# Performance work log

Measured on AMD Instinct MI355X. Metric: run time of the kernel, lower is better.

The kernel has to match this reference:

```python
import jax, jax.numpy as jnp
import numpy as np

D = 512; H = 8; DFF = 2048; S1 = 1024; S2 = 512; B = 8; EPS = 1e-5


def setup_inputs() -> dict:
    key = jax.random.key(0)
    ks = jax.random.split(key, 10)
    def w(k, shape):
        return jax.random.normal(k, shape, dtype=jnp.float32) * 0.02
    return {
        "rna_embed": jax.random.normal(ks[0], (S1, B, D), dtype=jnp.float32),
        "protein_embed": jax.random.normal(ks[1], (S2, B, D), dtype=jnp.float32),
        # self-attention params (torch MHA packed in_proj)
        "Wqkv_s": w(ks[2], (3 * D, D)), "bqkv_s": jnp.zeros((3 * D,), jnp.float32),
        "Wo_s": w(ks[3], (D, D)), "bo_s": jnp.zeros((D,), jnp.float32),
        # cross-attention params
        "Wqkv_c": w(ks[4], (3 * D, D)), "bqkv_c": jnp.zeros((3 * D,), jnp.float32),
        "Wo_c": w(ks[5], (D, D)), "bo_c": jnp.zeros((D,), jnp.float32),
        # FFN params
        "W1": w(ks[6], (DFF, D)), "b1": jnp.zeros((DFF,), jnp.float32),
        "W2": w(ks[7], (D, DFF)), "b2": jnp.zeros((D,), jnp.float32),
        # LayerNorm params: norm0_1, norm1_1, norm1_2, norm2
        "g0": jnp.ones((D,), jnp.float32), "be0": jnp.zeros((D,), jnp.float32),
        "g11": jnp.ones((D,), jnp.float32), "be11": jnp.zeros((D,), jnp.float32),
        "g12": jnp.ones((D,), jnp.float32), "be12": jnp.zeros((D,), jnp.float32),
        "g2": jnp.ones((D,), jnp.float32), "be2": jnp.zeros((D,), jnp.float32),
    }


def _layernorm(x, g, b):
    m = jnp.mean(x, axis=-1, keepdims=True)
    v = jnp.mean(jnp.square(x - m), axis=-1, keepdims=True)
    return (x - m) * jax.lax.rsqrt(v + EPS) * g + b


def _mha(xq, xkv, Wqkv, bqkv, Wo, bo):
    # xq: (Sq, B, D), xkv: (Sk, B, D)
    Wq, Wk, Wv = jnp.split(Wqkv, 3, axis=0)
    bq, bk, bv = jnp.split(bqkv, 3)
    hd = D // H
    scale = 1.0 / np.sqrt(hd).astype(np.float32)
    q = (xq @ Wq.T + bq).reshape(xq.shape[0], -1, H, hd)   # (Sq,B,H,hd)
    k = (xkv @ Wk.T + bk).reshape(xkv.shape[0], -1, H, hd)  # (Sk,B,H,hd)
    v = (xkv @ Wv.T + bv).reshape(xkv.shape[0], -1, H, hd)
    scores = jnp.einsum('qbhd,kbhd->bhqk', q, k) * scale    # (B,H,Sq,Sk)
    attn = jax.nn.softmax(scores, axis=-1)
    o = jnp.einsum('bhqk,kbhd->qbhd', attn, v).reshape(xq.shape[0], -1, D)
    return o @ Wo.T + bo


def reference(rna_embed, protein_embed, Wqkv_s, bqkv_s, Wo_s, bo_s,
              Wqkv_c, bqkv_c, Wo_c, bo_c, W1, b1, W2, b2,
              g0, be0, g11, be11, g12, be12, g2, be2):
    x1 = rna_embed
    # pre-norm self-attention
    h = _layernorm(x1, g0, be0)
    x1 = x1 + _mha(h, h, Wqkv_s, bqkv_s, Wo_s, bo_s)
    # pre-norm cross-attention (queries from x1, keys/values from protein)
    x1 = x1 + _mha(_layernorm(x1, g11, be11), _layernorm(protein_embed, g12, be12),
                   Wqkv_c, bqkv_c, Wo_c, bo_c)
    # pre-norm FFN
    h = _layernorm(x1, g2, be2)
    x1 = x1 + (jax.nn.relu(h @ W1.T + b1) @ W2.T + b2)
    return x1
```

## Files before the change

kernel.cpp:

```cpp
#include <hip/hip_runtime.h>

typedef unsigned short u16;
typedef unsigned int u32;
typedef u16 u16x8 __attribute__((ext_vector_type(8)));
typedef u16 u16x4 __attribute__((ext_vector_type(4)));
typedef short bfx8 __attribute__((ext_vector_type(8)));
typedef float f32x4 __attribute__((ext_vector_type(4)));

#define AS1 __attribute__((address_space(1)))
#define AS3 __attribute__((address_space(3)))

__device__ __forceinline__ u16 f2bf(float f) {
  union { float f; u32 u; } c; c.f = f;
  u32 u = c.u;
  u += 0x7fffu + ((u >> 16) & 1u);
  return (u16)(u >> 16);
}

__device__ __forceinline__ u32 cvt_pk_bf16(float lo, float hi) {
  u32 r;
  asm("v_cvt_pk_bf16_f32 %0, %1, %2" : "=v"(r) : "v"(lo), "v"(hi));
  return r;
}

__device__ __forceinline__ float fexp2(float x) {
  float r;
  asm("v_exp_f32 %0, %1" : "=v"(r) : "v"(x));
  return r;
}

__device__ __forceinline__ void ln_row(const float* __restrict__ x,
                                       const float* __restrict__ g,
                                       const float* __restrict__ be,
                                       u16* __restrict__ out, int gw, int lane) {
  const float4* row = (const float4*)(x + (size_t)gw * 512);
  float4 a = row[2 * lane], b = row[2 * lane + 1];
  float s = a.x + a.y + a.z + a.w + b.x + b.y + b.z + b.w;
  float q = a.x*a.x + a.y*a.y + a.z*a.z + a.w*a.w + b.x*b.x + b.y*b.y + b.z*b.z + b.w*b.w;
#pragma unroll
  for (int m = 1; m < 64; m <<= 1) { s += __shfl_xor(s, m); q += __shfl_xor(q, m); }
  float mean = s * (1.f / 512.f);
  float var = q * (1.f / 512.f) - mean * mean;
  float rs = rsqrtf(var + 1e-5f);
  const float4* g4 = (const float4*)g;
  const float4* b4 = (const float4*)be;
  float4 ga = g4[2 * lane], gb = g4[2 * lane + 1];
  float4 ba = b4[2 * lane], bb = b4[2 * lane + 1];
  u16x8 o;
  o[0] = f2bf((a.x - mean) * rs * ga.x + ba.x);
  o[1] = f2bf((a.y - mean) * rs * ga.y + ba.y);
  o[2] = f2bf((a.z - mean) * rs * ga.z + ba.z);
  o[3] = f2bf((a.w - mean) * rs * ga.w + ba.w);
  o[4] = f2bf((b.x - mean) * rs * gb.x + bb.x);
  o[5] = f2bf((b.y - mean) * rs * gb.y + bb.y);
  o[6] = f2bf((b.z - mean) * rs * gb.z + bb.z);
  o[7] = f2bf((b.w - mean) * rs * gb.w + bb.w);
  ((u16x8*)(out + (size_t)gw * 512))[lane] = o;
}

__global__ __launch_bounds__(256) void cvtln_kernel(const float* __restrict__ a0, const float* __restrict__ a1,
                                                    const float* __restrict__ a2, const float* __restrict__ a3,
                                                    const float* __restrict__ a4, const float* __restrict__ a5,
                                                    u16* __restrict__ b0, u16* __restrict__ b1,
                                                    u16* __restrict__ b2, u16* __restrict__ b3,
                                                    u16* __restrict__ b4, u16* __restrict__ b5,
                                                    const float* __restrict__ x, const float* __restrict__ g,
                                                    const float* __restrict__ be, u16* __restrict__ lnout) {
  if (blockIdx.x < 4096) {
    int i = blockIdx.x * 256 + threadIdx.x;
    const float* s; u16* d; int off;
    if      (i < 196608) { s = a0; d = b0; off = i; }
    else if (i < 262144) { s = a1; d = b1; off = i - 196608; }
    else if (i < 458752) { s = a2; d = b2; off = i - 262144; }
    else if (i < 524288) { s = a3; d = b3; off = i - 458752; }
    else if (i < 786432) { s = a4; d = b4; off = i - 524288; }
    else                 { s = a5; d = b5; off = i - 786432; }
    float4 v = ((const float4*)s)[off];
    u16x4 o;
    o[0] = f2bf(v.x); o[1] = f2bf(v.y); o[2] = f2bf(v.z); o[3] = f2bf(v.w);
    ((u16x4*)d)[off] = o;
  } else {
    int gw = ((blockIdx.x - 4096) * 256 + threadIdx.x) >> 6;
    ln_row(x, g, be, lnout, gw, threadIdx.x & 63);
  }
}

__global__ __launch_bounds__(256) void ln_kernel(const float* __restrict__ x,
                                                 const float* __restrict__ g,
                                                 const float* __restrict__ be,
                                                 u16* __restrict__ out, int ntok) {
  int gw = (blockIdx.x * 256 + threadIdx.x) >> 6;
  if (gw >= ntok) return;
  ln_row(x, g, be, out, gw, threadIdx.x & 63);
}

__global__ __launch_bounds__(256) void ln2_kernel(const float* __restrict__ xa, const float* __restrict__ ga,
                                                  const float* __restrict__ ba, u16* __restrict__ oa,
                                                  const float* __restrict__ xb, const float* __restrict__ gb,
                                                  const float* __restrict__ bb, u16* __restrict__ ob) {
  int lane = threadIdx.x & 63;
  if (blockIdx.x < 2048) {
    int gw = (blockIdx.x * 256 + threadIdx.x) >> 6;
    ln_row(xa, ga, ba, oa, gw, lane);
  } else {
    int gw = ((blockIdx.x - 2048) * 256 + threadIdx.x) >> 6;
    ln_row(xb, gb, bb, ob, gw, lane);
  }
}

__global__ __launch_bounds__(256) void vt_kernel(const u16* __restrict__ vB, u16* __restrict__ vt,
                                                 int stride, int S) {
  __shared__ u16 lt[64 * 68];
  const int t = threadIdx.x;
  const int b = blockIdx.y, h = blockIdx.z;
  const int sr = t >> 3, dc = (t & 7) * 8;
#pragma unroll
  for (int p = 0; p < 2; ++p) {
    int s = blockIdx.x * 64 + sr + p * 32;
    u16x8 v = *(const u16x8*)(vB + (size_t)(s * 8 + b) * stride + h * 64 + dc);
    u16x4 lo, hi;
    lo[0]=v[0]; lo[1]=v[1]; lo[2]=v[2]; lo[3]=v[3];
    hi[0]=v[4]; hi[1]=v[5]; hi[2]=v[6]; hi[3]=v[7];
    *(u16x4*)&lt[(sr + p * 32) * 68 + dc] = lo;
    *(u16x4*)&lt[(sr + p * 32) * 68 + dc + 4] = hi;
  }
  __syncthreads();
#pragma unroll
  for (int p = 0; p < 2; ++p) {
    int d = sr + p * 32;
    u16x8 o;
#pragma unroll
    for (int e = 0; e < 8; ++e) o[e] = lt[(dc + e) * 68 + d];
    *(u16x8*)(vt + ((size_t)(b * 8 + h) * 64 + d) * S + blockIdx.x * 64 + dc) = o;
  }
}

template <int EPI, int BM, int BN, int MINW>
__global__ __launch_bounds__(512, MINW) void gemm8(const u16* __restrict__ A,
                                                   const u16* __restrict__ Bw,
                                                   const float* __restrict__ bias,
                                                   const float* __restrict__ res,
                                                   void* __restrict__ Cout,
                                                   int N, int M, int K) {
  constexpr int WCg = BN / 64;
  constexpr int WRg = 8 / WCg;
  constexpr int RPW = BM / WRg;
  constexpr int IM = RPW / 16;
  constexpr int LD = (BM + BN) / 64;
  __shared__ __align__(16) u16 lA[2][BM * 64];
  __shared__ __align__(16) u16 lB[2][BN * 64];
  const int tid = threadIdx.x;
  const int lane = tid & 63, w = tid >> 6;
  const int wr = w / WCg, wc = w % WCg;
  const int nwg = gridDim.x * gridDim.y;
  const int id = blockIdx.y * gridDim.x + blockIdx.x;
  const int swz = (id & 7) * (nwg >> 3) + (id >> 3);
  const int bn = (swz / gridDim.x) * BM;
  const int bm = (swz % gridDim.x) * BN;
  const int r15 = lane & 15, kg = lane >> 4;
  const int xr = (r15 & 7) << 4;

  f32x4 acc[IM][4] = {};

  const int lrw = tid >> 3;
  const int lcl = ((tid & 7) * 8) ^ ((lrw & 7) * 8);
  const u16* gA = A + (size_t)(bn + lrw) * K + lcl;
  const u16* gB = Bw + (size_t)(bm + lrw) * K + lcl;
  const int ldsbase = (w * 8) * 64;

#define STAGE8(buf, t) do {                                                               \
    _Pragma("unroll")                                                                     \
    for (int i_ = 0; i_ < BM / 64; ++i_)                                                  \
      __builtin_amdgcn_global_load_lds((AS1 u32*)(gA + (size_t)(i_ * 64) * K + (t) * 64), \
                                       (AS3 u32*)&lA[buf][i_ * 4096 + ldsbase], 16, 0, 0);\
    _Pragma("unroll")                                                                     \
    for (int i_ = 0; i_ < BN / 64; ++i_)                                                  \
      __builtin_amdgcn_global_load_lds((AS1 u32*)(gB + (size_t)(i_ * 64) * K + (t) * 64), \
                                       (AS3 u32*)&lB[buf][i_ * 4096 + ldsbase], 16, 0, 0);\
  } while (0)

  const int nk = K >> 6;
  STAGE8(0, 0);
  for (int t = 0; t < nk; ++t) {
    const int cur = t & 1;
    if (t + 1 < nk) {
      STAGE8(cur ^ 1, t + 1);
      if constexpr (LD == 4) asm volatile("s_waitcnt vmcnt(4)" ::: "memory");
      else                   asm volatile("s_waitcnt vmcnt(8)" ::: "memory");
    } else {
      asm volatile("s_waitcnt vmcnt(0)" ::: "memory");
    }
    __builtin_amdgcn_sched_barrier(0);
    __builtin_amdgcn_s_barrier();
    __builtin_amdgcn_sched_barrier(0);

    const char* Ac = (const char*)lA[cur];
    const char* Bc = (const char*)lB[cur];
    __builtin_amdgcn_s_setprio(1);
#pragma unroll
    for (int kk = 0; kk < 2; ++kk) {
      bfx8 a[IM], b[4];
#pragma unroll
      for (int i = 0; i < IM; ++i)
        a[i] = *(const bfx8*)(Ac + (wr * RPW + i * 16 + r15) * 128 + ((kk * 64 + kg * 16) ^ xr));
#pragma unroll
      for (int j = 0; j < 4; ++j)
        b[j] = *(const bfx8*)(Bc + (wc * 64 + j * 16 + r15) * 128 + ((kk * 64 + kg * 16) ^ xr));
#pragma unroll
      for (int i = 0; i < IM; ++i)
#pragma unroll
        for (int j = 0; j < 4; ++j)
          acc[i][j] = __builtin_amdgcn_mfma_f32_16x16x32_bf16(a[i], b[j], acc[i][j], 0, 0, 0);
    }
    __builtin_amdgcn_s_setprio(0);
    __builtin_amdgcn_sched_barrier(0);
    __builtin_amdgcn_s_barrier();
  }
#undef STAGE8

#pragma unroll
  for (int i = 0; i < IM; ++i) {
#pragma unroll
    for (int j = 0; j < 4; ++j) {
      int col = bm + wc * 64 + j * 16 + r15;
      float bv = bias[col];
#pragma unroll
      for (int r = 0; r < 4; ++r) {
        int row = bn + wr * RPW + i * 16 + kg * 4 + r;
        float v = acc[i][j][r] + bv;
        if (EPI == 1) v = fmaxf(v, 0.f);
        if (EPI == 2) {
          ((float*)Cout)[(size_t)row * M + col] = res[(size_t)row * M + col] + v;
        } else {
          ((u16*)Cout)[(size_t)row * M + col] = f2bf(v);
        }
      }
    }
  }
}

__global__ __launch_bounds__(512, 6) void attn_kernel(const u16* __restrict__ qB,
                                                      const u16* __restrict__ kB,
                                                      const u16* __restrict__ vtB,
                                                      u16* __restrict__ oB,
                                                      int qStride, int kvStride, int Sk) {
  __shared__ __align__(16) u16 lK[2][64 * 64];
  __shared__ __align__(16) u16 lVt[2][64 * 64];
  __shared__ __align__(16) u16 lP[8][16 * 64];
  const int tid = threadIdx.x, lane = tid & 63, w = tid >> 6;
  const int sid = blockIdx.x;
  const int h = sid & 7, b = (sid >> 3) & 7, qt = sid >> 6;
  const int r15 = lane & 15, kg = lane >> 4;
  const int srow = lane >> 3;
  const int sxcol = ((lane & 7) * 8) ^ (srow * 8);

  const int qs = qt * 128 + w * 16 + r15;
  const u16* qrow = qB + (size_t)(qs * 8 + b) * qStride + h * 64;
  bfx8 qf0 = *(const bfx8*)(qrow + kg * 8);
  bfx8 qf1 = *(const bfx8*)(qrow + 32 + kg * 8);

  const u16* vbase = vtB + ((size_t)(b * 8 + h) * 64) * Sk;
  const u16* kp0 = kB + ((size_t)(w * 8 + srow) * 8 + b) * kvStride + h * 64 + sxcol;
  const size_t kAdv = (size_t)64 * 8 * kvStride;
  const u16* vp0 = vbase + (size_t)(w * 8 + srow) * Sk + sxcol;

#define STAGE(buf, tt) do {                                                           \
    __builtin_amdgcn_global_load_lds((AS1 u32*)(kp0 + (size_t)(tt) * kAdv),           \
                                     (AS3 u32*)&lK[buf][(w * 8) * 64], 16, 0, 0);     \
    __builtin_amdgcn_global_load_lds((AS1 u32*)(vp0 + (size_t)(tt) * 64),             \
                                     (AS3 u32*)&lVt[buf][(w * 8) * 64], 16, 0, 0);    \
  } while (0)

  const int nt = Sk / 64;
  STAGE(0, 0);
  STAGE(1, 1);

  f32x4 oacc[4] = {};
  float mrow = -1e30f, lsum = 0.f;
  const float C2 = 0.125f * 1.44269504088896340736f;
  const int xr = (r15 & 7) << 4;
  char* myP = (char*)lP[w];

  for (int t = 0; t < nt; ++t) {
    int cur = t & 1;
    if (t < nt - 1) { asm volatile("s_waitcnt vmcnt(2)" ::: "memory"); }
    else            { asm volatile("s_waitcnt vmcnt(0)" ::: "memory"); }
    __builtin_amdgcn_sched_barrier(0);
    __builtin_amdgcn_s_barrier();
    __builtin_amdgcn_sched_barrier(0);

    const char* Kc = (const char*)lK[cur];
    f32x4 st[4] = {};
    __builtin_amdgcn_s_setprio(1);
#pragma unroll
    for (int j = 0; j < 4; ++j) {
      const char* kp = Kc + (j * 16 + r15) * 128;
      bfx8 kf0 = *(const bfx8*)(kp + ((kg * 16) ^ xr));
      bfx8 kf1 = *(const bfx8*)(kp + ((64 + kg * 16) ^ xr));
      st[j] = __builtin_amdgcn_mfma_f32_16x16x32_bf16(kf0, qf0, st[j], 0, 0, 0);
      st[j] = __builtin_amdgcn_mfma_f32_16x16x32_bf16(kf1, qf1, st[j], 0, 0, 0);
    }
    __builtin_amdgcn_s_setprio(0);

    float m0 = fmaxf(fmaxf(fmaxf(st[0][0], st[0][1]), fmaxf(st[0][2], st[0][3])),
                     fmaxf(fmaxf(st[1][0], st[1][1]), fmaxf(st[1][2], st[1][3])));
    float m1 = fmaxf(fmaxf(fmaxf(st[2][0], st[2][1]), fmaxf(st[2][2], st[2][3])),
                     fmaxf(fmaxf(st[3][0], st[3][1]), fmaxf(st[3][2], st[3][3])));
    m0 = fmaxf(m0, m1);
    m0 = fmaxf(m0, __shfl_xor(m0, 16));
    m0 = fmaxf(m0, __shfl_xor(m0, 32));

    float mn = fmaxf(mrow, m0);
    float corr = fexp2((mrow - mn) * C2);
    mrow = mn;
    float bc = -mn * C2;

    float p[4][4];
#pragma unroll
    for (int j = 0; j < 4; ++j)
#pragma unroll
      for (int r = 0; r < 4; ++r)
        p[j][r] = fexp2(fmaf(st[j][r], C2, bc));

    float ps = ((p[0][0] + p[0][1]) + (p[0][2] + p[0][3]))
             + ((p[1][0] + p[1][1]) + (p[1][2] + p[1][3]))
             + ((p[2][0] + p[2][1]) + (p[2][2] + p[2][3]))
             + ((p[3][0] + p[3][1]) + (p[3][2] + p[3][3]));
    ps += __shfl_xor(ps, 16);
    ps += __shfl_xor(ps, 32);
    lsum = lsum * corr + ps;
#pragma unroll
    for (int jd = 0; jd < 4; ++jd)
#pragma unroll
      for (int r = 0; r < 4; ++r) oacc[jd][r] *= corr;

#pragma unroll
    for (int j = 0; j < 4; ++j)
#pragma unroll
      for (int h2 = 0; h2 < 2; ++h2) {
        u32 pk = cvt_pk_bf16(p[j][2 * h2], p[j][2 * h2 + 1]);
        int k0b = (j * 16 + kg * 4 + 2 * h2) * 2;
        *(u32*)(myP + r15 * 128 + (k0b ^ xr)) = pk;
      }

    const char* Vc = (const char*)lVt[cur];
    __builtin_amdgcn_s_setprio(1);
#pragma unroll
    for (int s2 = 0; s2 < 2; ++s2) {
      bfx8 ptf = *(const bfx8*)(myP + r15 * 128 + ((s2 * 64 + kg * 16) ^ xr));
#pragma unroll
      for (int jd = 0; jd < 4; ++jd) {
        const char* vp = Vc + (jd * 16 + r15) * 128;
        bfx8 vf = *(const bfx8*)(vp + ((s2 * 64 + kg * 16) ^ xr));
        oacc[jd] = __builtin_amdgcn_mfma_f32_16x16x32_bf16(vf, ptf, oacc[jd], 0, 0, 0);
      }
    }
    __builtin_amdgcn_s_setprio(0);

    __builtin_amdgcn_sched_barrier(0);
    __builtin_amdgcn_s_barrier();
    __builtin_amdgcn_sched_barrier(0);
    if (t + 2 < nt) STAGE(cur, t + 2);
  }
#undef STAGE

  float inv = 1.f / lsum;
  const int s = qt * 128 + w * 16 + r15;
  u16* orow = oB + (size_t)(s * 8 + b) * 512 + h * 64;
#pragma unroll
  for (int jd = 0; jd < 4; ++jd) {
    u32 p0 = cvt_pk_bf16(oacc[jd][0] * inv, oacc[jd][1] * inv);
    u32 p1 = cvt_pk_bf16(oacc[jd][2] * inv, oacc[jd][3] * inv);
    *(u32*)(orow + jd * 16 + kg * 4) = p0;
    *(u32*)(orow + jd * 16 + kg * 4 + 2) = p1;
  }
}

extern "C" void kernel_launch(void* const* d_in, const int* in_sizes, int n_in,
                              void* d_out, int out_size, void* d_ws, size_t ws_size,
                              hipStream_t stream) {
  const float* rna    = (const float*)d_in[0];
  const float* prot   = (const float*)d_in[1];
  const float* Wqkv_s = (const float*)d_in[2];
  const float* bqkv_s = (const float*)d_in[3];
  const float* Wo_s   = (const float*)d_in[4];
  const float* bo_s   = (const float*)d_in[5];
  const float* Wqkv_c = (const float*)d_in[6];
  const float* bqkv_c = (const float*)d_in[7];
  const float* Wo_c   = (const float*)d_in[8];
  const float* bo_c   = (const float*)d_in[9];
  const float* W1     = (const float*)d_in[10];
  const float* b1     = (const float*)d_in[11];
  const float* W2     = (const float*)d_in[12];
  const float* b2     = (const float*)d_in[13];
  const float* g0  = (const float*)d_in[14];
  const float* be0 = (const float*)d_in[15];
  const float* g11 = (const float*)d_in[16];
  const float* be11= (const float*)d_in[17];
  const float* g12 = (const float*)d_in[18];
  const float* be12= (const float*)d_in[19];
  const float* g2  = (const float*)d_in[20];
  const float* be2 = (const float*)d_in[21];
  float* out = (float*)d_out;

  u16* wbf      = (u16*)d_ws;
  u16* w_qkv_s  = wbf;
  u16* w_o_s    = wbf + 786432;
  u16* w_qkv_c  = wbf + 1048576;
  u16* w_o_c    = wbf + 1835008;
  u16* w_1      = wbf + 2097152;
  u16* w_2      = wbf + 3145728;
  u16* hbuf     = wbf + 4194304;
  u16* qkv      = hbuf + 4194304;
  u16* kvc      = qkv + 4194304;
  u16* attnO    = qkv + 12582912;
  u16* hp       = attnO + 4194304;
  u16* ffnmid   = qkv;

  cvtln_kernel<<<6144, 256, 0, stream>>>(Wqkv_s, Wo_s, Wqkv_c, Wo_c, W1, W2,
                                         w_qkv_s, w_o_s, w_qkv_c, w_o_c, w_1, w_2,
                                         rna, g0, be0, hbuf);

  gemm8<0, 256, 256, 2><<<dim3(6, 32), 512, 0, stream>>>(hbuf, w_qkv_s, bqkv_s, nullptr, qkv, 8192, 1536, 512);
  vt_kernel<<<dim3(16, 8, 8), 256, 0, stream>>>(qkv + 1024, hbuf, 1536, 1024);
  attn_kernel<<<512, 512, 0, stream>>>(qkv, qkv + 512, hbuf, attnO, 1536, 1536, 1024);
  gemm8<2, 128, 128, 4><<<dim3(4, 64), 512, 0, stream>>>(attnO, w_o_s, bo_s, rna, out, 8192, 512, 512);

  ln2_kernel<<<3072, 256, 0, stream>>>(out, g11, be11, hbuf, prot, g12, be12, hp);
  gemm8<0, 128, 128, 4><<<dim3(4, 64), 512, 0, stream>>>(hbuf, w_qkv_c, bqkv_c, nullptr, qkv, 8192, 512, 512);
  gemm8<0, 128, 128, 4><<<dim3(8, 32), 512, 0, stream>>>(hp, w_qkv_c + 512 * 512, bqkv_c + 512, nullptr, kvc, 4096, 1024, 512);
  vt_kernel<<<dim3(8, 8, 8), 256, 0, stream>>>(kvc + 512, hp, 1024, 512);
  attn_kernel<<<512, 512, 0, stream>>>(qkv, kvc, hp, attnO, 512, 1024, 512);
  gemm8<2, 128, 128, 4><<<dim3(4, 64), 512, 0, stream>>>(attnO, w_o_c, bo_c, out, out, 8192, 512, 512);

  ln_kernel<<<2048, 256, 0, stream>>>(out, g2, be2, hbuf, 8192);
  gemm8<1, 256, 256, 2><<<dim3(8, 32), 512, 0, stream>>>(hbuf, w_1, b1, nullptr, ffnmid, 8192, 2048, 512);
  gemm8<2, 128, 128, 4><<<dim3(4, 64), 512, 0, stream>>>(ffnmid, w_2, b2, out, out, 8192, 512, 2048);
}
```

Baseline: 214.5 us.

## Process two KV tiles per attention iteration, lazy rescale, smaller GEMM tiles

```diff
diff --git a/kernel.cpp b/kernel.cpp
--- a/kernel.cpp
+++ b/kernel.cpp
@@ -185,8 +185,9 @@
     const int cur = t & 1;
     if (t + 1 < nk) {
       STAGE8(cur ^ 1, t + 1);
-      if constexpr (LD == 4) asm volatile("s_waitcnt vmcnt(4)" ::: "memory");
-      else                   asm volatile("s_waitcnt vmcnt(8)" ::: "memory");
+      if constexpr (LD == 3)      asm volatile("s_waitcnt vmcnt(3)" ::: "memory");
+      else if constexpr (LD == 4) asm volatile("s_waitcnt vmcnt(4)" ::: "memory");
+      else                        asm volatile("s_waitcnt vmcnt(8)" ::: "memory");
     } else {
       asm volatile("s_waitcnt vmcnt(0)" ::: "memory");
     }
@@ -239,13 +240,13 @@
   }
 }
 
-__global__ __launch_bounds__(512, 6) void attn_kernel(const u16* __restrict__ qB,
+__global__ __launch_bounds__(512, 4) void attn_kernel(const u16* __restrict__ qB,
                                                       const u16* __restrict__ kB,
                                                       const u16* __restrict__ vtB,
                                                       u16* __restrict__ oB,
                                                       int qStride, int kvStride, int Sk) {
-  __shared__ __align__(16) u16 lK[2][64 * 64];
-  __shared__ __align__(16) u16 lVt[2][64 * 64];
+  __shared__ __align__(16) u16 lK[4][64 * 64];
+  __shared__ __align__(16) u16 lVt[4][64 * 64];
   __shared__ __align__(16) u16 lP[8][16 * 64];
   const int tid = threadIdx.x, lane = tid & 63, w = tid >> 6;
   const int sid = blockIdx.x;
@@ -272,8 +273,8 @@
   } while (0)
 
   const int nt = Sk / 64;
-  STAGE(0, 0);
-  STAGE(1, 1);
+  const int np = nt >> 1;
+  STAGE(0, 0); STAGE(1, 1); STAGE(2, 2); STAGE(3, 3);
 
   f32x4 oacc[4] = {};
   float mrow = -1e30f, lsum = 0.f;
@@ -281,86 +282,126 @@
   const int xr = (r15 & 7) << 4;
   char* myP = (char*)lP[w];
 
-  for (int t = 0; t < nt; ++t) {
-    int cur = t & 1;
-    if (t < nt - 1) { asm volatile("s_waitcnt vmcnt(2)" ::: "memory"); }
+  for (int i = 0; i < np; ++i) {
+    const int ba = (2 * i) & 3, bb = (2 * i + 1) & 3;
+    if (i + 1 < np) { asm volatile("s_waitcnt vmcnt(4)" ::: "memory"); }
     else            { asm volatile("s_waitcnt vmcnt(0)" ::: "memory"); }
     __builtin_amdgcn_sched_barrier(0);
     __builtin_amdgcn_s_barrier();
     __builtin_amdgcn_sched_barrier(0);
 
-    const char* Kc = (const char*)lK[cur];
-    f32x4 st[4] = {};
+    const char* Ka = (const char*)lK[ba];
+    const char* Kb = (const char*)lK[bb];
+    f32x4 sa[4] = {}, sb[4] = {};
     __builtin_amdgcn_s_setprio(1);
 #pragma unroll
     for (int j = 0; j < 4; ++j) {
-      const char* kp = Kc + (j * 16 + r15) * 128;
-      bfx8 kf0 = *(const bfx8*)(kp + ((kg * 16) ^ xr));
-      bfx8 kf1 = *(const bfx8*)(kp + ((64 + kg * 16) ^ xr));
-      st[j] = __builtin_amdgcn_mfma_f32_16x16x32_bf16(kf0, qf0, st[j], 0, 0, 0);
-      st[j] = __builtin_amdgcn_mfma_f32_16x16x32_bf16(kf1, qf1, st[j], 0, 0, 0);
+      const char* kpa = Ka + (j * 16 + r15) * 128;
+      bfx8 ka0 = *(const bfx8*)(kpa + ((kg * 16) ^ xr));
+      bfx8 ka1 = *(const bfx8*)(kpa + ((64 + kg * 16) ^ xr));
+      sa[j] = __builtin_amdgcn_mfma_f32_16x16x32_bf16(ka0, qf0, sa[j], 0, 0, 0);
+      sa[j] = __builtin_amdgcn_mfma_f32_16x16x32_bf16(ka1, qf1, sa[j], 0, 0, 0);
+    }
+#pragma unroll
+    for (int j = 0; j < 4; ++j) {
+      const char* kpb = Kb + (j * 16 + r15) * 128;
+      bfx8 kb0 = *(const bfx8*)(kpb + ((kg * 16) ^ xr));
+      bfx8 kb1 = *(const bfx8*)(kpb + ((64 + kg * 16) ^ xr));
+      sb[j] = __builtin_amdgcn_mfma_f32_16x16x32_bf16(kb0, qf0, sb[j], 0, 0, 0);
+      sb[j] = __builtin_amdgcn_mfma_f32_16x16x32_bf16(kb1, qf1, sb[j], 0, 0, 0);
     }
     __builtin_amdgcn_s_setprio(0);
 
-    float m0 = fmaxf(fmaxf(fmaxf(st[0][0], st[0][1]), fmaxf(st[0][2], st[0][3])),
-                     fmaxf(fmaxf(st[1][0], st[1][1]), fmaxf(st[1][2], st[1][3])));
-    float m1 = fmaxf(fmaxf(fmaxf(st[2][0], st[2][1]), fmaxf(st[2][2], st[2][3])),
-                     fmaxf(fmaxf(st[3][0], st[3][1]), fmaxf(st[3][2], st[3][3])));
-    m0 = fmaxf(m0, m1);
+    float ma = fmaxf(fmaxf(fmaxf(sa[0][0], sa[0][1]), fmaxf(sa[0][2], sa[0][3])),
+                     fmaxf(fmaxf(sa[1][0], sa[1][1]), fmaxf(sa[1][2], sa[1][3])));
+    float ma2 = fmaxf(fmaxf(fmaxf(sa[2][0], sa[2][1]), fmaxf(sa[2][2], sa[2][3])),
+                      fmaxf(fmaxf(sa[3][0], sa[3][1]), fmaxf(sa[3][2], sa[3][3])));
+    float mb = fmaxf(fmaxf(fmaxf(sb[0][0], sb[0][1]), fmaxf(sb[0][2], sb[0][3])),
+                     fmaxf(fmaxf(sb[1][0], sb[1][1]), fmaxf(sb[1][2], sb[1][3])));
+    float mb2 = fmaxf(fmaxf(fmaxf(sb[2][0], sb[2][1]), fmaxf(sb[2][2], sb[2][3])),
+                      fmaxf(fmaxf(sb[3][0], sb[3][1]), fmaxf(sb[3][2], sb[3][3])));
+    float m0 = fmaxf(fmaxf(ma, ma2), fmaxf(mb, mb2));
     m0 = fmaxf(m0, __shfl_xor(m0, 16));
     m0 = fmaxf(m0, __shfl_xor(m0, 32));
 
-    float mn = fmaxf(mrow, m0);
-    float corr = fexp2((mrow - mn) * C2);
-    mrow = mn;
-    float bc = -mn * C2;
-
-    float p[4][4];
+    if (!__all(m0 <= mrow + 16.0f)) {
+      float mn = fmaxf(mrow, m0);
+      float corr = fexp2((mrow - mn) * C2);
+      mrow = mn;
+      lsum *= corr;
+#pragma unroll
+      for (int jd = 0; jd < 4; ++jd)
+#pragma unroll
+        for (int r = 0; r < 4; ++r) oacc[jd][r] *= corr;
+    }
+    float bc = -mrow * C2;
+
+    float pa[4][4], pb[4][4];
 #pragma unroll
     for (int j = 0; j < 4; ++j)
 #pragma unroll
-      for (int r = 0; r < 4; ++r)
-        p[j][r] = fexp2(fmaf(st[j][r], C2, bc));
-
-    float ps = ((p[0][0] + p[0][1]) + (p[0][2] + p[0][3]))
-             + ((p[1][0] + p[1][1]) + (p[1][2] + p[1][3]))
-             + ((p[2][0] + p[2][1]) + (p[2][2] + p[2][3]))
-             + ((p[3][0] + p[3][1]) + (p[3][2] + p[3][3]));
+      for (int r = 0; r < 4; ++r) {
+        pa[j][r] = fexp2(fmaf(sa[j][r], C2, bc));
+        pb[j][r] = fexp2(fmaf(sb[j][r], C2, bc));
+      }
+
+    float ps = 0.f;
+#pragma unroll
+    for (int j = 0; j < 4; ++j)
+#pragma unroll
+      for (int r = 0; r < 4; ++r) ps += pa[j][r] + pb[j][r];
     ps += __shfl_xor(ps, 16);
     ps += __shfl_xor(ps, 32);
-    lsum = lsum * corr + ps;
-#pragma unroll
-    for (int jd = 0; jd < 4; ++jd)
-#pragma unroll
-      for (int r = 0; r < 4; ++r) oacc[jd][r] *= corr;
+    lsum += ps;
 
 #pragma unroll
     for (int j = 0; j < 4; ++j)
 #pragma unroll
       for (int h2 = 0; h2 < 2; ++h2) {
-        u32 pk = cvt_pk_bf16(p[j][2 * h2], p[j][2 * h2 + 1]);
+        u32 pk = cvt_pk_bf16(pa[j][2 * h2], pa[j][2 * h2 + 1]);
         int k0b = (j * 16 + kg * 4 + 2 * h2) * 2;
         *(u32*)(myP + r15 * 128 + (k0b ^ xr)) = pk;
       }
-
-    const char* Vc = (const char*)lVt[cur];
+    const char* Va = (const char*)lVt[ba];
     __builtin_amdgcn_s_setprio(1);
 #pragma unroll
     for (int s2 = 0; s2 < 2; ++s2) {
       bfx8 ptf = *(const bfx8*)(myP + r15 * 128 + ((s2 * 64 + kg * 16) ^ xr));
 #pragma unroll
       for (int jd = 0; jd < 4; ++jd) {
-        const char* vp = Vc + (jd * 16 + r15) * 128;
+        const char* vp = Va + (jd * 16 + r15) * 128;
         bfx8 vf = *(const bfx8*)(vp + ((s2 * 64 + kg * 16) ^ xr));
         oacc[jd] = __builtin_amdgcn_mfma_f32_16x16x32_bf16(vf, ptf, oacc[jd], 0, 0, 0);
       }
     }
     __builtin_amdgcn_s_setprio(0);
 
+#pragma unroll
+    for (int j = 0; j < 4; ++j)
+#pragma unroll
+      for (int h2 = 0; h2 < 2; ++h2) {
+        u32 pk = cvt_pk_bf16(pb[j][2 * h2], pb[j][2 * h2 + 1]);
+        int k0b = (j * 16 + kg * 4 + 2 * h2) * 2;
+        *(u32*)(myP + r15 * 128 + (k0b ^ xr)) = pk;
+      }
+    const char* Vb = (const char*)lVt[bb];
+    __builtin_amdgcn_s_setprio(1);
+#pragma unroll
+    for (int s2 = 0; s2 < 2; ++s2) {
+      bfx8 ptf = *(const bfx8*)(myP + r15 * 128 + ((s2 * 64 + kg * 16) ^ xr));
+#pragma unroll
+      for (int jd = 0; jd < 4; ++jd) {
+        const char* vp = Vb + (jd * 16 + r15) * 128;
+        bfx8 vf = *(const bfx8*)(vp + ((s2 * 64 + kg * 16) ^ xr));
+        oacc[jd] = __builtin_amdgcn_mfma_f32_16x16x32_bf16(vf, ptf, oacc[jd], 0, 0, 0);
+      }
+    }
+    __builtin_amdgcn_s_setprio(0);
+
     __builtin_amdgcn_sched_barrier(0);
     __builtin_amdgcn_s_barrier();
     __builtin_amdgcn_sched_barrier(0);
-    if (t + 2 < nt) STAGE(cur, t + 2);
+    if (2 * i + 4 < nt) { STAGE(ba, 2 * i + 4); STAGE(bb, 2 * i + 5); }
   }
 #undef STAGE
 
@@ -424,16 +465,16 @@
   gemm8<0, 256, 256, 2><<<dim3(6, 32), 512, 0, stream>>>(hbuf, w_qkv_s, bqkv_s, nullptr, qkv, 8192, 1536, 512);
   vt_kernel<<<dim3(16, 8, 8), 256, 0, stream>>>(qkv + 1024, hbuf, 1536, 1024);
   attn_kernel<<<512, 512, 0, stream>>>(qkv, qkv + 512, hbuf, attnO, 1536, 1536, 1024);
-  gemm8<2, 128, 128, 4><<<dim3(4, 64), 512, 0, stream>>>(attnO, w_o_s, bo_s, rna, out, 8192, 512, 512);
+  gemm8<2, 64, 128, 6><<<dim3(4, 128), 512, 0, stream>>>(attnO, w_o_s, bo_s, rna, out, 8192, 512, 512);
 
   ln2_kernel<<<3072, 256, 0, stream>>>(out, g11, be11, hbuf, prot, g12, be12, hp);
-  gemm8<0, 128, 128, 4><<<dim3(4, 64), 512, 0, stream>>>(hbuf, w_qkv_c, bqkv_c, nullptr, qkv, 8192, 512, 512);
-  gemm8<0, 128, 128, 4><<<dim3(8, 32), 512, 0, stream>>>(hp, w_qkv_c + 512 * 512, bqkv_c + 512, nullptr, kvc, 4096, 1024, 512);
+  gemm8<0, 64, 128, 6><<<dim3(4, 128), 512, 0, stream>>>(hbuf, w_qkv_c, bqkv_c, nullptr, qkv, 8192, 512, 512);
+  gemm8<0, 64, 128, 6><<<dim3(8, 64), 512, 0, stream>>>(hp, w_qkv_c + 512 * 512, bqkv_c + 512, nullptr, kvc, 4096, 1024, 512);
   vt_kernel<<<dim3(8, 8, 8), 256, 0, stream>>>(kvc + 512, hp, 1024, 512);
   attn_kernel<<<512, 512, 0, stream>>>(qkv, kvc, hp, attnO, 512, 1024, 512);
-  gemm8<2, 128, 128, 4><<<dim3(4, 64), 512, 0, stream>>>(attnO, w_o_c, bo_c, out, out, 8192, 512, 512);
+  gemm8<2, 64, 128, 6><<<dim3(4, 128), 512, 0, stream>>>(attnO, w_o_c, bo_c, out, out, 8192, 512, 512);
 
   ln_kernel<<<2048, 256, 0, stream>>>(out, g2, be2, hbuf, 8192);
   gemm8<1, 256, 256, 2><<<dim3(8, 32), 512, 0, stream>>>(hbuf, w_1, b1, nullptr, ffnmid, 8192, 2048, 512);
-  gemm8<2, 128, 128, 4><<<dim3(4, 64), 512, 0, stream>>>(ffnmid, w_2, b2, out, out, 8192, 512, 2048);
-}
+  gemm8<2, 64, 128, 6><<<dim3(4, 128), 512, 0, stream>>>(ffnmid, w_2, b2, out, out, 8192, 512, 2048);
+}
```

Result: faster. 204.3 us (-4.8%).
